# Kernel tuning notes

Hardware: AMD Instinct MI355X
Metric: run time of the kernel (lower is better)

The kernel has to match this reference:

```python
import jax, jax.numpy as jnp
import numpy as np

N_NODES = 100000
N_EDGES = 1200000
DIM = 64
MAX_DEG = 64
NUM_LAB = 16
BN_EPS = 1e-5


def _lrelu(x):
    return jax.nn.leaky_relu(x, negative_slope=0.01)


def _bn(x, g, b):
    # BatchNorm1d in training mode: batch statistics over node axis
    m = x.mean(axis=0)
    v = x.var(axis=0)
    return (x - m) * jax.lax.rsqrt(v + BN_EPS) * g + b


def _gin_layer(h, src, dst, n, w1, b1, w2, b2, eps, g, b):
    # GINConv: (1+eps)*x_i + sum_{j in N(i)} x_j, then MLP (lin_lrelu_lin), BN, LeakyReLU
    agg = jax.ops.segment_sum(h[src], dst, num_segments=n)
    x = (1.0 + eps) * h + agg
    x = _lrelu(x @ w1 + b1) @ w2 + b2
    return _lrelu(_bn(x, g, b))


def setup_inputs() -> dict:
    key = jax.random.key(0)
    ks = jax.random.split(key, 16)
    s = 0.05
    inp = {
        'node_deg': jax.random.randint(ks[0], (N_NODES,), 0, MAX_DEG + 1, dtype=jnp.int32),
        'node_lab': jax.random.randint(ks[1], (N_NODES,), 0, NUM_LAB, dtype=jnp.int32),
        'edge_index': jax.random.randint(ks[2], (2, N_EDGES), 0, N_NODES, dtype=jnp.int32),
        'emb_deg': jax.random.normal(ks[3], (MAX_DEG + 1, DIM), jnp.float32) * s,
        'emb_lab': jax.random.normal(ks[4], (NUM_LAB, DIM), jnp.float32) * s,
        'l0_w1': jax.random.normal(ks[5], (2 * DIM, 2 * DIM), jnp.float32) * s,
        'l0_b1': jnp.zeros((2 * DIM,), jnp.float32),
        'l0_w2': jax.random.normal(ks[6], (2 * DIM, DIM), jnp.float32) * s,
        'l0_b2': jnp.zeros((DIM,), jnp.float32),
        'l0_eps': jnp.zeros((1,), jnp.float32),
        'bn0_g': jnp.ones((DIM,), jnp.float32),
        'bn0_b': jnp.zeros((DIM,), jnp.float32),
        'l1_w1': jax.random.normal(ks[7], (DIM, DIM), jnp.float32) * s,
        'l1_b1': jnp.zeros((DIM,), jnp.float32),
        'l1_w2': jax.random.normal(ks[8], (DIM, DIM), jnp.float32) * s,
        'l1_b2': jnp.zeros((DIM,), jnp.float32),
        'l1_eps': jnp.zeros((1,), jnp.float32),
        'bn1_g': jnp.ones((DIM,), jnp.float32),
        'bn1_b': jnp.zeros((DIM,), jnp.float32),
        'fc_w1': jax.random.normal(ks[9], (4 * DIM, DIM), jnp.float32) * s,
        'fc_b1': jnp.zeros((DIM,), jnp.float32),
        'fc_bn_g': jnp.ones((DIM,), jnp.float32),
        'fc_bn_b': jnp.zeros((DIM,), jnp.float32),
        'fc_w2': jax.random.normal(ks[10], (DIM, 1), jnp.float32) * s,
        'fc_b2': jnp.zeros((1,), jnp.float32),
    }
    return inp


def reference(node_deg, node_lab, edge_index, emb_deg, emb_lab,
              l0_w1, l0_b1, l0_w2, l0_b2, l0_eps, bn0_g, bn0_b,
              l1_w1, l1_b1, l1_w2, l1_b2, l1_eps, bn1_g, bn1_b,
              fc_w1, fc_b1, fc_bn_g, fc_bn_b, fc_w2, fc_b2):
    n = node_deg.shape[0]
    src, dst = edge_index[0], edge_index[1]
    # embedding concat: [N, 2*DIM]
    h0 = jnp.concatenate([emb_deg[node_deg], emb_lab[node_lab]], axis=1)
    h1 = _gin_layer(h0, src, dst, n, l0_w1, l0_b1, l0_w2, l0_b2, l0_eps[0], bn0_g, bn0_b)
    h2 = _gin_layer(h1, src, dst, n, l1_w1, l1_b1, l1_w2, l1_b2, l1_eps[0], bn1_g, bn1_b)
    x = jnp.concatenate([h0, h1, h2], axis=1)  # [N, 256]
    x = _lrelu(_bn(x @ fc_w1 + fc_b1, fc_bn_g, fc_bn_b))
    out = jax.nn.sigmoid(x @ fc_w2 + fc_b2)
    return out.squeeze(-1)  # [N]
```

## Files before the change

### kernel.cpp

```cpp
#include <hip/hip_runtime.h>

#define N_NODES 100000
#define N_EDGES 1200000
#define NCLS 81
#define NBKT 196
#define BCAP 8192
#define NCHK 293
#define NGBLK 1563

typedef unsigned short u16;
typedef unsigned char u8;
typedef unsigned int u32;
typedef unsigned long long u64;
typedef short bf16x8 __attribute__((ext_vector_type(8)));
typedef float f32x4 __attribute__((ext_vector_type(4)));

__device__ __forceinline__ float b2f(u16 u) {
  union { u32 i; float f; } v; v.i = ((u32)u) << 16; return v.f;
}
__device__ __forceinline__ u16 f2b(float f) {
  union { float f; u32 i; } v; v.f = f;
  u32 x = v.i;
  return (u16)((x + 0x7fffu + ((x >> 16) & 1u)) >> 16);
}
__device__ __forceinline__ void up2(u32 w, float& lo, float& hi) {
  union { u32 u; float f; } a, b;
  a.u = w << 16; b.u = w & 0xffff0000u;
  lo = a.f; hi = b.f;
}
__device__ __forceinline__ float lrelu(float x) { return x > 0.f ? x : 0.01f * x; }

__device__ __forceinline__ bool is_f32(const u16* emb) {
  int lane = threadIdx.x & 63;
  u32 e0 = (emb[lane * 2] >> 7) & 0xFF;
  u32 e1 = (emb[lane * 2 + 1] >> 7) & 0xFF;
  return __ballot((e0 >= 0x90) || (e1 >= 0x90)) != 0ull;
}

__device__ __forceinline__ float rdr(const void* p, int i, bool f32m) {
  return f32m ? ((const float*)p)[i] : b2f(((const u16*)p)[i]);
}

#define P_EMBD 0
#define P_EMBL 4160
#define P_W1A  5184
#define P_B1A  21568
#define P_W2A  21696
#define P_B2A  29888
#define P_EPS0 29952
#define P_G0   29953
#define P_BB0  30017
#define P_LW1  30081
#define P_LB1  34177
#define P_LW2  34241
#define P_LB2  38337
#define P_EPS1 38401
#define P_G1   38402
#define P_BB1  38466
#define P_FW1  38530
#define P_FB1  54914
#define P_FG   54978
#define P_FBB  55042
#define P_FW2  55106
#define P_FB2  55170
#define P_TOT  55171

struct CvtAll {
  const void* src[22];
  int cnt[22];
  int off[22];
};

struct RawPtrs {
  const void* embD;
  const void* embL;
  const void* w1r;
  const void* w2r;
  const void* lw1r;
  const void* lw2r;
  const void* fwr;
};

__global__ void k_init(CvtAll a, RawPtrs rw, const u16* __restrict__ embRaw,
                       float* __restrict__ P, float* __restrict__ W1p,
                       float* __restrict__ Efc, u16* __restrict__ bp,
                       u16* __restrict__ wpB, u32* __restrict__ gcur) {
  bool f32m = is_f32(embRaw);
  int tid = threadIdx.x;
  if (blockIdx.y < 22) {
    if (blockIdx.y == 0 && blockIdx.x == 0 && tid < NBKT) gcur[tid] = 0;
    int seg = blockIdx.y;
    int i = blockIdx.x * 256 + tid;
    if (i < a.cnt[seg]) {
      float v = f32m ? ((const float*)a.src[seg])[i] : b2f(((const u16*)a.src[seg])[i]);
      P[a.off[seg] + i] = v;
    }
    return;
  }
  int idx = blockIdx.x * 256 + tid;
  if (idx < NCLS * 128) {
    int c = idx >> 7, h = idx & 127;
    float s = 0.f;
    if (c < 65) {
      for (int k = 0; k < 64; ++k)
        s = fmaf(rdr(rw.embD, c * 64 + k, f32m), rdr(rw.w1r, k * 128 + h, f32m), s);
    } else {
      for (int k = 0; k < 64; ++k)
        s = fmaf(rdr(rw.embL, (c - 65) * 64 + k, f32m), rdr(rw.w1r, (64 + k) * 128 + h, f32m), s);
    }
    W1p[idx] = s;
    return;
  }
  if (idx < NCLS * 128 + NCLS * 64) {
    int r = idx - NCLS * 128;
    int c = r >> 6, o = r & 63;
    float s = 0.f;
    if (c < 65) {
      for (int k = 0; k < 64; ++k)
        s = fmaf(rdr(rw.embD, c * 64 + k, f32m), rdr(rw.fwr, k * 64 + o, f32m), s);
    } else {
      for (int k = 0; k < 64; ++k)
        s = fmaf(rdr(rw.embL, (c - 65) * 64 + k, f32m), rdr(rw.fwr, (64 + k) * 64 + o, f32m), s);
    }
    Efc[r] = s;
    return;
  }
  if (idx < NCLS * 128 + NCLS * 64 + 24576) {
    int pidx = idx - (NCLS * 128 + NCLS * 64);
    int seg, rel;
    if (pidx < 8192)       { seg = 0; rel = pidx; }
    else if (pidx < 12288) { seg = 1; rel = pidx - 8192; }
    else if (pidx < 16384) { seg = 2; rel = pidx - 12288; }
    else                   { seg = 3; rel = pidx - 16384; }
    const void* srcs[4] = {rw.w2r, rw.lw1r, rw.lw2r, rw.fwr};
    const int addoff[4] = {0, 0, 0, 128 * 64};
    const int KBs[4] = {4, 2, 2, 4};
    int j = rel & 7, lane = (rel >> 3) & 63, rest = rel >> 9;
    int kb = rest % KBs[seg], nt = rest / KBs[seg];
    int k = kb * 32 + (lane >> 4) * 8 + j;
    int n = nt * 16 + (lane & 15);
    bp[pidx] = f2b(rdr(srcs[seg], addoff[seg] + k * 64 + n, f32m));
    return;
  }
  int p2 = idx - (NCLS * 128 + NCLS * 64 + 24576);
  if (p2 >= 12288) return;
  int j = p2 & 7, lane = (p2 >> 3) & 63, rest = p2 >> 9;
  int kb = rest % 3, nt = rest / 3;
  int c = kb * 32 + (lane >> 4) * 8 + j;
  int n = nt * 16 + (lane & 15);
  float s = 0.f;
  if (c < NCLS) {
    if (c < 65) {
      for (int k = 0; k < 64; ++k)
        s = fmaf(rdr(rw.embD, c * 64 + k, f32m), rdr(rw.w1r, k * 128 + n, f32m), s);
    } else {
      for (int k = 0; k < 64; ++k)
        s = fmaf(rdr(rw.embL, (c - 65) * 64 + k, f32m), rdr(rw.w1r, (64 + k) * 128 + n, f32m), s);
    }
  }
  wpB[p2] = (c < NCLS) ? f2b(s) : 0;
}

__global__ __launch_bounds__(256) void k_bsort(const int* __restrict__ edge,
                                               const int* __restrict__ ndeg,
                                               const int* __restrict__ nlab,
                                               u32* __restrict__ gcur,
                                               u64* __restrict__ e2) {
  __shared__ u32 cnt[NBKT], rbase[NBKT];
  __shared__ u32 slo[4096], shi[4096];
  for (int i = threadIdx.x; i < NBKT; i += 256) cnt[i] = 0;
  __syncthreads();
  int base = blockIdx.x * 4096;
  for (int i = threadIdx.x; i < 4096; i += 256) {
    int e = base + i;
    if (e < N_EDGES) {
      int s = edge[e], d = edge[N_EDGES + e];
      slo[i] = ((u32)s << 11) | ((u32)ndeg[s] << 4) | (u32)nlab[s];
      shi[i] = (u32)d;
      atomicAdd(&cnt[(u32)d >> 9], 1u);
    } else shi[i] = 0xFFFFFFFFu;
  }
  __syncthreads();
  for (int i = threadIdx.x; i < NBKT; i += 256) {
    u32 c = cnt[i];
    rbase[i] = c ? atomicAdd(&gcur[i], c) : 0u;
    cnt[i] = 0;
  }
  __syncthreads();
  for (int i = threadIdx.x; i < 4096; i += 256) {
    u32 d = shi[i];
    if (d == 0xFFFFFFFFu) continue;
    u32 b = d >> 9;
    u32 pos = rbase[b] + atomicAdd(&cnt[b], 1u);
    e2[(size_t)b * BCAP + pos] = ((u64)d << 32) | (u64)slo[i];
  }
}

__global__ __launch_bounds__(512) void k_csrh(const u64* __restrict__ e2,
                                              const u32* __restrict__ gcur,
                                              const u16* __restrict__ wpB,
                                              const float* __restrict__ W1p,
                                              const float* __restrict__ P,
                                              const int* __restrict__ ndeg,
                                              const int* __restrict__ nlab,
                                              u32* __restrict__ row_ptr,
                                              u32* __restrict__ einfo,
                                              u16* __restrict__ hmid) {
  __shared__ u32 l[512], cur[512], gl[NBKT];
  __shared__ u32 h32[512 * 24];
  __shared__ u32 sbase;
  int b = blockIdx.x, tid = threadIdx.x;
  if (tid < NBKT) gl[tid] = gcur[tid];
  l[tid] = 0;
  for (int i = tid; i < 512 * 24; i += 512) h32[i] = 0;
  __syncthreads();
  if (tid == 0) {
    u32 s = 0;
    for (int i = 0; i < b; ++i) s += gl[i];
    sbase = s;
  }
  __syncthreads();
  u32 cnt = gl[b];
  const u64* src = e2 + (size_t)b * BCAP;
  for (u32 e = tid; e < cnt; e += 512)
    atomicAdd(&l[(u32)(src[e] >> 32) & 511u], 1u);
  __syncthreads();
  u32 v = l[tid];
  for (int off = 1; off < 512; off <<= 1) {
    u32 a = (tid >= off) ? l[tid - off] : 0u;
    __syncthreads();
    l[tid] += a;
    __syncthreads();
  }
  u32 pos0 = sbase + l[tid] - v;
  cur[tid] = pos0;
  int nn = b * 512 + tid;
  if (nn <= N_NODES) row_ptr[nn] = pos0;
  __syncthreads();
  for (u32 e = tid; e < cnt; e += 512) {
    u64 r = src[e];
    u32 dl = (u32)(r >> 32) & 511u;
    u32 lo = (u32)r;
    u32 pos = atomicAdd(&cur[dl], 1u);
    einfo[pos] = lo;
    u32 c1 = (lo >> 4) & 0x7Fu, c2 = 65u + (lo & 15u);
    atomicAdd(&h32[dl * 24 + (c1 >> 2)], 1u << ((c1 & 3u) * 8));
    atomicAdd(&h32[dl * 24 + (c2 >> 2)], 1u << ((c2 & 3u) * 8));
  }
  __syncthreads();
  const u8* h = (const u8*)h32;
  int wid = tid >> 6, lane = tid & 63;
  int row = lane & 15, q = lane >> 4;
  float onep = 1.f + P[P_EPS0];
  const bf16x8* bp = (const bf16x8*)wpB;
#pragma unroll 1
  for (int t = wid; t < 32; t += 8) {
    int m0 = b * 512 + t * 16;
    if (m0 >= N_NODES) break;
    f32x4 acc[8];
#pragma unroll
    for (int nt = 0; nt < 8; ++nt) {
      float bb = P[P_B1A + nt * 16 + row];
      acc[nt][0] = bb; acc[nt][1] = bb; acc[nt][2] = bb; acc[nt][3] = bb;
    }
    const u8* ar = h + (t * 16 + row) * 96 + q * 8;
#pragma unroll
    for (int kb = 0; kb < 3; ++kb) {
      bf16x8 af;
#pragma unroll
      for (int j = 0; j < 8; ++j) af[j] = (short)f2b((float)ar[kb * 32 + j]);
#pragma unroll
      for (int nt = 0; nt < 8; ++nt) {
        bf16x8 bf = bp[(nt * 3 + kb) * 64 + lane];
        acc[nt] = __builtin_amdgcn_mfma_f32_16x16x32_bf16(af, bf, acc[nt], 0, 0, 0);
      }
    }
#pragma unroll
    for (int r = 0; r < 4; ++r) {
      int m = m0 + q * 4 + r;
      if (m >= N_NODES) continue;
      const float* wd = W1p + ndeg[m] * 128;
      const float* wl = W1p + (65 + nlab[m]) * 128;
#pragma unroll
      for (int nt = 0; nt < 8; ++nt) {
        int cc = nt * 16 + row;
        float vv = acc[nt][r] + onep * (wd[cc] + wl[cc]);
        hmid[(size_t)m * 128 + cc] = f2b(lrelu(vv));
      }
    }
  }
}

__global__ void k_sr(const float* __restrict__ pbuf, float* __restrict__ statsOut) {
  __shared__ float l[256];
  int c = blockIdx.x;
  float s = 0.f;
  for (int r = threadIdx.x; r < NGBLK; r += 256) s += pbuf[(size_t)r * 128 + c];
  l[threadIdx.x] = s;
  __syncthreads();
  for (int off = 128; off > 0; off >>= 1) {
    if (threadIdx.x < off) l[threadIdx.x] += l[threadIdx.x + off];
    __syncthreads();
  }
  if (threadIdx.x == 0) statsOut[c] = l[0];
}

template <int KB, int LDA, int BIASOFF>
__global__ __launch_bounds__(256) void k_gemm(const u16* __restrict__ A,
                                              const u16* __restrict__ Bp,
                                              const float* __restrict__ P,
                                              float* __restrict__ pbuf,
                                              u16* __restrict__ C) {
  __shared__ float lsum[4][64], lsq[4][64];
  int wid = threadIdx.x >> 6, lane = threadIdx.x & 63;
  int m0 = (blockIdx.x * 4 + wid) * 16;
  bool act = m0 < N_NODES;
  int row = lane & 15, q = lane >> 4;
  float ss[4] = {0.f, 0.f, 0.f, 0.f}, qq[4] = {0.f, 0.f, 0.f, 0.f};
  if (act) {
    const u16* ap = A + (size_t)(m0 + row) * LDA + q * 8;
    const bf16x8* bp = (const bf16x8*)Bp;
    f32x4 acc[4];
#pragma unroll
    for (int nt = 0; nt < 4; ++nt) {
      float b = (BIASOFF >= 0) ? P[BIASOFF + nt * 16 + row] : 0.f;
      acc[nt][0] = b; acc[nt][1] = b; acc[nt][2] = b; acc[nt][3] = b;
    }
#pragma unroll
    for (int kb = 0; kb < KB; ++kb) {
      bf16x8 af = *(const bf16x8*)(ap + kb * 32);
#pragma unroll
      for (int nt = 0; nt < 4; ++nt) {
        bf16x8 bf = bp[(nt * KB + kb) * 64 + lane];
        acc[nt] = __builtin_amdgcn_mfma_f32_16x16x32_bf16(af, bf, acc[nt], 0, 0, 0);
      }
    }
#pragma unroll
    for (int nt = 0; nt < 4; ++nt) {
      float s = 0.f, z = 0.f;
#pragma unroll
      for (int r = 0; r < 4; ++r) {
        int m = m0 + q * 4 + r;
        u16 bv = f2b(acc[nt][r]);
        C[(size_t)m * 64 + nt * 16 + row] = bv;
        float v = b2f(bv);
        s += v; z = fmaf(v, v, z);
      }
      s += __shfl_xor(s, 16, 64); s += __shfl_xor(s, 32, 64);
      z += __shfl_xor(z, 16, 64); z += __shfl_xor(z, 32, 64);
      ss[nt] = s; qq[nt] = z;
    }
  }
  if (lane < 16) {
#pragma unroll
    for (int nt = 0; nt < 4; ++nt) {
      lsum[wid][nt * 16 + lane] = ss[nt];
      lsq[wid][nt * 16 + lane] = qq[nt];
    }
  }
  __syncthreads();
  int t = threadIdx.x;
  if (t < 64)
    pbuf[(size_t)blockIdx.x * 128 + t] = lsum[0][t] + lsum[1][t] + lsum[2][t] + lsum[3][t];
  else if (t < 128) {
    int c = t - 64;
    pbuf[(size_t)blockIdx.x * 128 + t] = lsq[0][c] + lsq[1][c] + lsq[2][c] + lsq[3][c];
  }
}

__global__ __launch_bounds__(256) void k_gemm_bn(const u16* __restrict__ A,
                                                 const u16* __restrict__ Bp,
                                                 const float* __restrict__ P,
                                                 const float* __restrict__ stats,
                                                 u16* __restrict__ C) {
  int wid = threadIdx.x >> 6, lane = threadIdx.x & 63;
  int m0 = (blockIdx.x * 4 + wid) * 16;
  if (m0 >= N_NODES) return;
  int row = lane & 15, q = lane >> 4;
  const float invN = 1.f / (float)N_NODES;
  float sc[16], sh[16];
#pragma unroll
  for (int kb = 0; kb < 2; ++kb)
#pragma unroll
    for (int j = 0; j < 8; ++j) {
      int f = kb * 32 + q * 8 + j;
      float mm = stats[f] * invN;
      float var = fmaxf(stats[64 + f] * invN - mm * mm, 0.f);
      float inv = rsqrtf(var + 1e-5f);
      float s = inv * P[P_G0 + f];
      sc[kb * 8 + j] = s;
      sh[kb * 8 + j] = P[P_BB0 + f] - mm * s;
    }
  const u16* ap = A + (size_t)(m0 + row) * 64 + q * 8;
  const bf16x8* bp = (const bf16x8*)Bp;
  f32x4 acc[4];
#pragma unroll
  for (int nt = 0; nt < 4; ++nt) {
    acc[nt][0] = 0.f; acc[nt][1] = 0.f; acc[nt][2] = 0.f; acc[nt][3] = 0.f;
  }
#pragma unroll
  for (int kb = 0; kb < 2; ++kb) {
    uint4 raw = *(const uint4*)(ap + kb * 32);
    u32 rw[4] = {raw.x, raw.y, raw.z, raw.w};
    bf16x8 af;
#pragma unroll
    for (int p = 0; p < 4; ++p) {
      float lo, hi;
      up2(rw[p], lo, hi);
      float y0 = lrelu(fmaf(sc[kb * 8 + 2 * p], lo, sh[kb * 8 + 2 * p]));
      float y1 = lrelu(fmaf(sc[kb * 8 + 2 * p + 1], hi, sh[kb * 8 + 2 * p + 1]));
      af[2 * p] = (short)f2b(y0);
      af[2 * p + 1] = (short)f2b(y1);
    }
#pragma unroll
    for (int nt = 0; nt < 4; ++nt) {
      bf16x8 bf = bp[(nt * 2 + kb) * 64 + lane];
      acc[nt] = __builtin_amdgcn_mfma_f32_16x16x32_bf16(af, bf, acc[nt], 0, 0, 0);
    }
  }
#pragma unroll
  for (int nt = 0; nt < 4; ++nt)
#pragma unroll
    for (int r = 0; r < 4; ++r) {
      int m = m0 + q * 4 + r;
      C[(size_t)m * 64 + nt * 16 + row] = f2b(acc[nt][r]);
    }
}

__global__ __launch_bounds__(256) void k_agg_gemm(const u32* __restrict__ rp,
                                                  const u32* __restrict__ einfo,
                                                  const u16* __restrict__ g1,
                                                  const u16* __restrict__ Bp,
                                                  const float* __restrict__ P,
                                                  float* __restrict__ pbuf,
                                                  u16* __restrict__ C) {
  __shared__ float lsum[4][64], lsq[4][64];
  __shared__ u16 As[4][16][72];
  int wid = threadIdx.x >> 6, lane = threadIdx.x & 63;
  int m0 = (blockIdx.x * 4 + wid) * 16;
  bool act = m0 < N_NODES;
  int row = lane & 15, q = lane >> 4;
  float ss[4] = {0.f, 0.f, 0.f, 0.f}, qq[4] = {0.f, 0.f, 0.f, 0.f};
  if (act) {
    int grp = lane >> 4;
    int fo = (lane & 15) * 4;
    float onep = 1.f + P[P_EPS1];
    u32 rpv = 0;
    if (lane <= 16) rpv = rp[m0 + lane];
#pragma unroll 1
    for (int r = 0; r < 16; ++r) {
      int n = m0 + r;
      u32 st = (u32)__shfl((int)rpv, r, 64);
      u32 en = (u32)__shfl((int)rpv, r + 1, 64);
      u32 m = en - st;
      u32 myidx = (u32)n;
      if (lane < (int)m) myidx = einfo[st + lane] >> 11;
      u32 mm = m < 64u ? m : 64u;
      float a0 = 0.f, a1 = 0.f, a2 = 0.f, a3 = 0.f;
      for (u32 k = 0; k < mm; k += 16) {
#pragma unroll
        for (int bb = 0; bb < 4; ++bb) {
          u32 e = k + (u32)(bb * 4 + grp);
          u32 src = (u32)__shfl((int)myidx, (int)e, 64);
          if (e < mm) {
            uint2 v = *(const uint2*)(g1 + (size_t)src * 64 + fo);
            float l0, h0, l1, h1;
            up2(v.x, l0, h0);
            up2(v.y, l1, h1);
            a0 += l0; a1 += h0; a2 += l1; a3 += h1;
          }
        }
      }
      a0 += __shfl_xor(a0, 16, 64); a0 += __shfl_xor(a0, 32, 64);
      a1 += __shfl_xor(a1, 16, 64); a1 += __shfl_xor(a1, 32, 64);
      a2 += __shfl_xor(a2, 16, 64); a2 += __shfl_xor(a2, 32, 64);
      a3 += __shfl_xor(a3, 16, 64); a3 += __shfl_xor(a3, 32, 64);
      for (u32 k = 64; k < m; ++k) {
        u32 src = einfo[st + k] >> 11;
        uint2 v = *(const uint2*)(g1 + (size_t)src * 64 + fo);
        float l0, h0, l1, h1;
        up2(v.x, l0, h0);
        up2(v.y, l1, h1);
        a0 += l0; a1 += h0; a2 += l1; a3 += h1;
      }
      uint2 sv = *(const uint2*)(g1 + (size_t)n * 64 + fo);
      float s0, s1, s2, s3;
      up2(sv.x, s0, s1);
      up2(sv.y, s2, s3);
      float r0 = P[P_LB1 + fo + 0] + fmaf(onep, s0, a0);
      float r1 = P[P_LB1 + fo + 1] + fmaf(onep, s1, a1);
      float r2 = P[P_LB1 + fo + 2] + fmaf(onep, s2, a2);
      float r3 = P[P_LB1 + fo + 3] + fmaf(onep, s3, a3);
      if (lane < 16) {
        uint2 o;
        o.x = ((u32)f2b(lrelu(r0))) | (((u32)f2b(lrelu(r1))) << 16);
        o.y = ((u32)f2b(lrelu(r2))) | (((u32)f2b(lrelu(r3))) << 16);
        *(uint2*)&As[wid][r][fo] = o;
      }
    }
    const u16* ap = &As[wid][row][q * 8];
    const bf16x8* bp = (const bf16x8*)Bp;
    f32x4 acc[4];
#pragma unroll
    for (int nt = 0; nt < 4; ++nt) {
      float b = P[P_LB2 + nt * 16 + row];
      acc[nt][0] = b; acc[nt][1] = b; acc[nt][2] = b; acc[nt][3] = b;
    }
#pragma unroll
    for (int kb = 0; kb < 2; ++kb) {
      bf16x8 af = *(const bf16x8*)(ap + kb * 32);
#pragma unroll
      for (int nt = 0; nt < 4; ++nt) {
        bf16x8 bf = bp[(nt * 2 + kb) * 64 + lane];
        acc[nt] = __builtin_amdgcn_mfma_f32_16x16x32_bf16(af, bf, acc[nt], 0, 0, 0);
      }
    }
#pragma unroll
    for (int nt = 0; nt < 4; ++nt) {
      float s = 0.f, z = 0.f;
#pragma unroll
      for (int r = 0; r < 4; ++r) {
        int m = m0 + q * 4 + r;
        u16 bv = f2b(acc[nt][r]);
        C[(size_t)m * 64 + nt * 16 + row] = bv;
        float v = b2f(bv);
        s += v; z = fmaf(v, v, z);
      }
      s += __shfl_xor(s, 16, 64); s += __shfl_xor(s, 32, 64);
      z += __shfl_xor(z, 16, 64); z += __shfl_xor(z, 32, 64);
      ss[nt] = s; qq[nt] = z;
    }
  }
  if (lane < 16) {
#pragma unroll
    for (int nt = 0; nt < 4; ++nt) {
      lsum[wid][nt * 16 + lane] = ss[nt];
      lsq[wid][nt * 16 + lane] = qq[nt];
    }
  }
  __syncthreads();
  int t = threadIdx.x;
  if (t < 64)
    pbuf[(size_t)blockIdx.x * 128 + t] = lsum[0][t] + lsum[1][t] + lsum[2][t] + lsum[3][t];
  else if (t < 128) {
    int c = t - 64;
    pbuf[(size_t)blockIdx.x * 128 + t] = lsq[0][c] + lsq[1][c] + lsq[2][c] + lsq[3][c];
  }
}

__global__ __launch_bounds__(256) void k_gemm_fc1bn(const u16* __restrict__ t0,
                                                    const u16* __restrict__ t1,
                                                    const u16* __restrict__ Bp,
                                                    const float* __restrict__ P,
                                                    const float* __restrict__ stats,
                                                    float* __restrict__ pbuf,
                                                    const int* __restrict__ ndeg,
                                                    const int* __restrict__ nlab,
                                                    const float* __restrict__ Efc,
                                                    u16* __restrict__ C) {
  __shared__ float lsum[4][64], lsq[4][64];
  int wid = threadIdx.x >> 6, lane = threadIdx.x & 63;
  int m0 = (blockIdx.x * 4 + wid) * 16;
  bool act = m0 < N_NODES;
  int row = lane & 15, q = lane >> 4;
  float ss[4] = {0.f, 0.f, 0.f, 0.f}, qq[4] = {0.f, 0.f, 0.f, 0.f};
  if (act) {
    const float invN = 1.f / (float)N_NODES;
    float sc[32], sh[32];
#pragma unroll
    for (int h = 0; h < 2; ++h) {
      const float* st = stats + h * 128;
      int gof = h ? P_G1 : P_G0, bof = h ? P_BB1 : P_BB0;
#pragma unroll
      for (int kb = 0; kb < 2; ++kb)
#pragma unroll
        for (int j = 0; j < 8; ++j) {
          int f = kb * 32 + q * 8 + j;
          float mm = st[f] * invN;
          float var = fmaxf(st[64 + f] * invN - mm * mm, 0.f);
          float inv = rsqrtf(var + 1e-5f);
          float s = inv * P[gof + f];
          sc[h * 16 + kb * 8 + j] = s;
          sh[h * 16 + kb * 8 + j] = P[bof + f] - mm * s;
        }
    }
    const u16* a0 = t0 + (size_t)(m0 + row) * 64 + q * 8;
    const u16* a1 = t1 + (size_t)(m0 + row) * 64 + q * 8;
    const bf16x8* bp = (const bf16x8*)Bp;
    f32x4 acc[4];
#pragma unroll
    for (int nt = 0; nt < 4; ++nt) {
      float b = P[P_FB1 + nt * 16 + row];
      acc[nt][0] = b; acc[nt][1] = b; acc[nt][2] = b; acc[nt][3] = b;
    }
#pragma unroll
    for (int kb = 0; kb < 4; ++kb) {
      const u16* src = (kb < 2) ? (a0 + kb * 32) : (a1 + (kb - 2) * 32);
      int ci = (kb < 2) ? kb * 8 : 16 + (kb - 2) * 8;
      uint4 raw = *(const uint4*)src;
      u32 rw[4] = {raw.x, raw.y, raw.z, raw.w};
      bf16x8 af;
#pragma unroll
      for (int p = 0; p < 4; ++p) {
        float lo, hi;
        up2(rw[p], lo, hi);
        float y0 = lrelu(fmaf(sc[ci + 2 * p], lo, sh[ci + 2 * p]));
        float y1 = lrelu(fmaf(sc[ci + 2 * p + 1], hi, sh[ci + 2 * p + 1]));
        af[2 * p] = (short)f2b(y0);
        af[2 * p + 1] = (short)f2b(y1);
      }
#pragma unroll
      for (int nt = 0; nt < 4; ++nt) {
        bf16x8 bf = bp[(nt * 4 + kb) * 64 + lane];
        acc[nt] = __builtin_amdgcn_mfma_f32_16x16x32_bf16(af, bf, acc[nt], 0, 0, 0);
      }
    }
    float es[4][4];
#pragma unroll
    for (int r = 0; r < 4; ++r) {
      int m = m0 + q * 4 + r;
      int dn = ndeg[m], ln = 65 + nlab[m];
#pragma unroll
      for (int nt = 0; nt < 4; ++nt) {
        int cc = nt * 16 + row;
        es[r][nt] = acc[nt][r] + Efc[dn * 64 + cc] + Efc[ln * 64 + cc];
      }
    }
#pragma unroll
    for (int nt = 0; nt < 4; ++nt) {
      float s = 0.f, z = 0.f;
#pragma unroll
      for (int r = 0; r < 4; ++r) {
        int m = m0 + q * 4 + r;
        u16 bv = f2b(es[r][nt]);
        C[(size_t)m * 64 + nt * 16 + row] = bv;
        float v = b2f(bv);
        s += v; z = fmaf(v, v, z);
      }
      s += __shfl_xor(s, 16, 64); s += __shfl_xor(s, 32, 64);
      z += __shfl_xor(z, 16, 64); z += __shfl_xor(z, 32, 64);
      ss[nt] = s; qq[nt] = z;
    }
  }
  if (lane < 16) {
#pragma unroll
    for (int nt = 0; nt < 4; ++nt) {
      lsum[wid][nt * 16 + lane] = ss[nt];
      lsq[wid][nt * 16 + lane] = qq[nt];
    }
  }
  __syncthreads();
  int t = threadIdx.x;
  if (t < 64)
    pbuf[(size_t)blockIdx.x * 128 + t] = lsum[0][t] + lsum[1][t] + lsum[2][t] + lsum[3][t];
  else if (t < 128) {
    int c = t - 64;
    pbuf[(size_t)blockIdx.x * 128 + t] = lsq[0][c] + lsq[1][c] + lsq[2][c] + lsq[3][c];
  }
}

__global__ void k_fc2(const u16* __restrict__ t, const float* __restrict__ stats,
                      const float* __restrict__ P, const u16* __restrict__ embRaw,
                      void* __restrict__ out) {
  bool f32m = is_f32(embRaw);
  int n = blockIdx.x * blockDim.x + threadIdx.x;
  if (n >= N_NODES) return;
  float z = P[P_FB2];
  const float invN = 1.f / (float)N_NODES;
  const u16* tn = t + (size_t)n * 64;
#pragma unroll 1
  for (int f = 0; f < 64; ++f) {
    float m = stats[f] * invN;
    float var = fmaxf(stats[64 + f] * invN - m * m, 0.f);
    float inv = rsqrtf(var + 1e-5f);
    float y = (b2f(tn[f]) - m) * inv * P[P_FG + f] + P[P_FBB + f];
    y = lrelu(y);
    z = fmaf(y, P[P_FW2 + f], z);
  }
  float s = 1.f / (1.f + expf(-z));
  if (!(fabsf(z) < 1e30f)) s = 0.25f;
  if (f32m) ((float*)out)[n] = s;
  else      ((u16*)out)[n] = f2b(s);
}

extern "C" void kernel_launch(void* const* d_in, const int* in_sizes, int n_in,
                              void* d_out, int out_size, void* d_ws, size_t ws_size,
                              hipStream_t stream) {
  const int* node_deg = (const int*)d_in[0];
  const int* node_lab = (const int*)d_in[1];
  const int* edge     = (const int*)d_in[2];
  const u16* embRaw   = (const u16*)d_in[3];
  (void)in_sizes; (void)n_in; (void)out_size; (void)ws_size;

  char* base = (char*)d_ws;
  size_t off = 0;
  auto alloc = [&](size_t bytes) -> void* {
    void* p = base + off;
    off += (bytes + 15) & ~(size_t)15;
    return p;
  };
  float* Pb    = (float*)alloc((size_t)P_TOT * 4);
  float* stats = (float*)alloc(384 * 4);
  u32* gcur    = (u32*)alloc(NBKT * 4);
  float* W1p   = (float*)alloc(NCLS * 128 * 4);
  float* Efc   = (float*)alloc(NCLS * 64 * 4);
  u16* bpack   = (u16*)alloc(24576 * 2);
  u16* wpB     = (u16*)alloc(12288 * 2);
  u32* row_ptr = (u32*)alloc((size_t)(N_NODES + 1) * 4);
  float* pbuf  = (float*)alloc((size_t)NGBLK * 128 * 4);
  u32* einfo   = (u32*)alloc((size_t)N_EDGES * 4);
  u64* e2      = (u64*)alloc((size_t)NBKT * BCAP * 8);
  void* arena  = alloc((size_t)N_NODES * 128 * 2);
  u16* t0      = (u16*)alloc((size_t)N_NODES * 64 * 2);
  u16* t1      = (u16*)alloc((size_t)N_NODES * 64 * 2);
  u16* t2      = (u16*)alloc((size_t)N_NODES * 64 * 2);
  u16* hmid = (u16*)arena;
  u16* g1   = (u16*)arena;
  u16* Bp_w2a = bpack;
  u16* Bp_lw1 = bpack + 8192;
  u16* Bp_lw2 = bpack + 12288;
  u16* Bp_fw1 = bpack + 16384;

  CvtAll ca;
  const int srcidx[22] = {3, 4, 5, 6, 7, 8, 9, 10, 11, 12, 13, 14, 15, 16, 17, 18, 19, 20, 21, 22, 23, 24};
  const int cnts[22]   = {4160, 1024, 16384, 128, 8192, 64, 1, 64, 64, 4096, 64, 4096, 64, 1, 64, 64, 16384, 64, 64, 64, 64, 1};
  const int offs[22]   = {P_EMBD, P_EMBL, P_W1A, P_B1A, P_W2A, P_B2A, P_EPS0, P_G0, P_BB0,
                          P_LW1, P_LB1, P_LW2, P_LB2, P_EPS1, P_G1, P_BB1,
                          P_FW1, P_FB1, P_FG, P_FBB, P_FW2, P_FB2};
  for (int i = 0; i < 22; ++i) { ca.src[i] = d_in[srcidx[i]]; ca.cnt[i] = cnts[i]; ca.off[i] = offs[i]; }
  RawPtrs rw;
  rw.embD = d_in[3]; rw.embL = d_in[4]; rw.w1r = d_in[5]; rw.w2r = d_in[7];
  rw.lw1r = d_in[12]; rw.lw2r = d_in[14]; rw.fwr = d_in[19];

  k_init<<<dim3(205, 23), 256, 0, stream>>>(ca, rw, embRaw, Pb, W1p, Efc, bpack, wpB, gcur);

  k_bsort<<<NCHK, 256, 0, stream>>>(edge, node_deg, node_lab, gcur, e2);

  k_csrh<<<NBKT, 512, 0, stream>>>(e2, gcur, wpB, W1p, Pb, node_deg, node_lab,
                                   row_ptr, einfo, hmid);

  const int GEMM_GRID = NGBLK;

  k_gemm<4, 128, P_B2A><<<GEMM_GRID, 256, 0, stream>>>(hmid, Bp_w2a, Pb, pbuf, t0);
  k_sr<<<128, 256, 0, stream>>>(pbuf, stats);

  k_gemm_bn<<<GEMM_GRID, 256, 0, stream>>>(t0, Bp_lw1, Pb, stats, g1);
  k_agg_gemm<<<GEMM_GRID, 256, 0, stream>>>(row_ptr, einfo, g1, Bp_lw2, Pb, pbuf, t1);
  k_sr<<<128, 256, 0, stream>>>(pbuf, stats + 128);

  k_gemm_fc1bn<<<GEMM_GRID, 256, 0, stream>>>(t0, t1, Bp_fw1, Pb, stats, pbuf,
                                              node_deg, node_lab, Efc, t2);
  k_sr<<<128, 256, 0, stream>>>(pbuf, stats + 256);
  k_fc2<<<(N_NODES + 255) / 256, 256, 0, stream>>>(t2, stats + 256, Pb, embRaw, d_out);
}
```

Baseline: 340.7 us.

## Parallelize second-layer aggregation to one wave per node; hoist BN constants in fc2

The layer-1 aggregation+GEMM kernel previously had each wave serially walk 16 nodes' neighbor lists. Now each 1024-thread block assigns one wave per node, writes the aggregated rows to shared memory, and a single wave runs the MFMA and emits per-block BN partial sums. This gives more memory-level parallelism for the gather but leaves 15 waves idle during the GEMM and quadruples the partial-stats rows k_sr must reduce. Separately, k_fc2 precomputes the BN scale/shift and weights into shared memory per block and loads rows as vectorized uint4 instead of recomputing stats per feature per node.

```diff
diff --git a/kernel.cpp b/kernel.cpp
--- a/kernel.cpp
+++ b/kernel.cpp
@@ -7,6 +7,7 @@
 #define BCAP 8192
 #define NCHK 293
 #define NGBLK 1563
+#define NAGG 6250
 
 typedef unsigned short u16;
 typedef unsigned char u8;
@@ -291,11 +292,12 @@
   }
 }
 
-__global__ void k_sr(const float* __restrict__ pbuf, float* __restrict__ statsOut) {
+__global__ void k_sr(const float* __restrict__ pbuf, float* __restrict__ statsOut,
+                     int nrows) {
   __shared__ float l[256];
   int c = blockIdx.x;
   float s = 0.f;
-  for (int r = threadIdx.x; r < NGBLK; r += 256) s += pbuf[(size_t)r * 128 + c];
+  for (int r = threadIdx.x; r < nrows; r += 256) s += pbuf[(size_t)r * 128 + c];
   l[threadIdx.x] = s;
   __syncthreads();
   for (int off = 128; off > 0; off >>= 1) {
@@ -427,124 +429,108 @@
     }
 }
 
-__global__ __launch_bounds__(256) void k_agg_gemm(const u32* __restrict__ rp,
-                                                  const u32* __restrict__ einfo,
-                                                  const u16* __restrict__ g1,
-                                                  const u16* __restrict__ Bp,
-                                                  const float* __restrict__ P,
-                                                  float* __restrict__ pbuf,
-                                                  u16* __restrict__ C) {
-  __shared__ float lsum[4][64], lsq[4][64];
-  __shared__ u16 As[4][16][72];
-  int wid = threadIdx.x >> 6, lane = threadIdx.x & 63;
-  int m0 = (blockIdx.x * 4 + wid) * 16;
-  bool act = m0 < N_NODES;
-  int row = lane & 15, q = lane >> 4;
-  float ss[4] = {0.f, 0.f, 0.f, 0.f}, qq[4] = {0.f, 0.f, 0.f, 0.f};
-  if (act) {
-    int grp = lane >> 4;
-    int fo = (lane & 15) * 4;
-    float onep = 1.f + P[P_EPS1];
-    u32 rpv = 0;
-    if (lane <= 16) rpv = rp[m0 + lane];
-#pragma unroll 1
-    for (int r = 0; r < 16; ++r) {
-      int n = m0 + r;
-      u32 st = (u32)__shfl((int)rpv, r, 64);
-      u32 en = (u32)__shfl((int)rpv, r + 1, 64);
-      u32 m = en - st;
-      u32 myidx = (u32)n;
-      if (lane < (int)m) myidx = einfo[st + lane] >> 11;
-      u32 mm = m < 64u ? m : 64u;
-      float a0 = 0.f, a1 = 0.f, a2 = 0.f, a3 = 0.f;
-      for (u32 k = 0; k < mm; k += 16) {
-#pragma unroll
-        for (int bb = 0; bb < 4; ++bb) {
-          u32 e = k + (u32)(bb * 4 + grp);
-          u32 src = (u32)__shfl((int)myidx, (int)e, 64);
-          if (e < mm) {
-            uint2 v = *(const uint2*)(g1 + (size_t)src * 64 + fo);
-            float l0, h0, l1, h1;
-            up2(v.x, l0, h0);
-            up2(v.y, l1, h1);
-            a0 += l0; a1 += h0; a2 += l1; a3 += h1;
-          }
-        }
-      }
-      a0 += __shfl_xor(a0, 16, 64); a0 += __shfl_xor(a0, 32, 64);
-      a1 += __shfl_xor(a1, 16, 64); a1 += __shfl_xor(a1, 32, 64);
-      a2 += __shfl_xor(a2, 16, 64); a2 += __shfl_xor(a2, 32, 64);
-      a3 += __shfl_xor(a3, 16, 64); a3 += __shfl_xor(a3, 32, 64);
-      for (u32 k = 64; k < m; ++k) {
-        u32 src = einfo[st + k] >> 11;
+__global__ __launch_bounds__(1024) void k_aggg(const u32* __restrict__ rp,
+                                               const u32* __restrict__ einfo,
+                                               const u16* __restrict__ g1,
+                                               const u16* __restrict__ Bp,
+                                               const float* __restrict__ P,
+                                               float* __restrict__ pbuf,
+                                               u16* __restrict__ C) {
+  __shared__ u16 As[16][72];
+  int lane = threadIdx.x & 63, wv = threadIdx.x >> 6;
+  int m0 = blockIdx.x * 16;
+  int n = m0 + wv;
+  u32 st = rp[n], en = rp[n + 1];
+  u32 m = en - st;
+  int grp = lane >> 4;
+  int fo = (lane & 15) * 4;
+  u32 myidx = (u32)n;
+  if (lane < (int)m) myidx = einfo[st + lane] >> 11;
+  u32 mm = m < 64u ? m : 64u;
+  float a0 = 0.f, a1 = 0.f, a2 = 0.f, a3 = 0.f;
+  for (u32 k = 0; k < mm; k += 16) {
+#pragma unroll
+    for (int bb = 0; bb < 4; ++bb) {
+      u32 e = k + (u32)(bb * 4 + grp);
+      u32 src = (u32)__shfl((int)myidx, (int)e, 64);
+      if (e < mm) {
         uint2 v = *(const uint2*)(g1 + (size_t)src * 64 + fo);
         float l0, h0, l1, h1;
         up2(v.x, l0, h0);
         up2(v.y, l1, h1);
         a0 += l0; a1 += h0; a2 += l1; a3 += h1;
       }
-      uint2 sv = *(const uint2*)(g1 + (size_t)n * 64 + fo);
-      float s0, s1, s2, s3;
-      up2(sv.x, s0, s1);
-      up2(sv.y, s2, s3);
-      float r0 = P[P_LB1 + fo + 0] + fmaf(onep, s0, a0);
-      float r1 = P[P_LB1 + fo + 1] + fmaf(onep, s1, a1);
-      float r2 = P[P_LB1 + fo + 2] + fmaf(onep, s2, a2);
-      float r3 = P[P_LB1 + fo + 3] + fmaf(onep, s3, a3);
-      if (lane < 16) {
-        uint2 o;
-        o.x = ((u32)f2b(lrelu(r0))) | (((u32)f2b(lrelu(r1))) << 16);
-        o.y = ((u32)f2b(lrelu(r2))) | (((u32)f2b(lrelu(r3))) << 16);
-        *(uint2*)&As[wid][r][fo] = o;
-      }
-    }
-    const u16* ap = &As[wid][row][q * 8];
-    const bf16x8* bp = (const bf16x8*)Bp;
-    f32x4 acc[4];
-#pragma unroll
-    for (int nt = 0; nt < 4; ++nt) {
-      float b = P[P_LB2 + nt * 16 + row];
-      acc[nt][0] = b; acc[nt][1] = b; acc[nt][2] = b; acc[nt][3] = b;
-    }
-#pragma unroll
-    for (int kb = 0; kb < 2; ++kb) {
-      bf16x8 af = *(const bf16x8*)(ap + kb * 32);
-#pragma unroll
-      for (int nt = 0; nt < 4; ++nt) {
-        bf16x8 bf = bp[(nt * 2 + kb) * 64 + lane];
-        acc[nt] = __builtin_amdgcn_mfma_f32_16x16x32_bf16(af, bf, acc[nt], 0, 0, 0);
-      }
-    }
-#pragma unroll
-    for (int nt = 0; nt < 4; ++nt) {
-      float s = 0.f, z = 0.f;
-#pragma unroll
-      for (int r = 0; r < 4; ++r) {
-        int m = m0 + q * 4 + r;
-        u16 bv = f2b(acc[nt][r]);
-        C[(size_t)m * 64 + nt * 16 + row] = bv;
-        float v = b2f(bv);
-        s += v; z = fmaf(v, v, z);
-      }
-      s += __shfl_xor(s, 16, 64); s += __shfl_xor(s, 32, 64);
-      z += __shfl_xor(z, 16, 64); z += __shfl_xor(z, 32, 64);
-      ss[nt] = s; qq[nt] = z;
-    }
-  }
+    }
+  }
+  a0 += __shfl_xor(a0, 16, 64); a0 += __shfl_xor(a0, 32, 64);
+  a1 += __shfl_xor(a1, 16, 64); a1 += __shfl_xor(a1, 32, 64);
+  a2 += __shfl_xor(a2, 16, 64); a2 += __shfl_xor(a2, 32, 64);
+  a3 += __shfl_xor(a3, 16, 64); a3 += __shfl_xor(a3, 32, 64);
+  for (u32 k = 64; k < m; ++k) {
+    u32 src = einfo[st + k] >> 11;
+    uint2 v = *(const uint2*)(g1 + (size_t)src * 64 + fo);
+    float l0, h0, l1, h1;
+    up2(v.x, l0, h0);
+    up2(v.y, l1, h1);
+    a0 += l0; a1 += h0; a2 += l1; a3 += h1;
+  }
+  float onep = 1.f + P[P_EPS1];
+  uint2 sv = *(const uint2*)(g1 + (size_t)n * 64 + fo);
+  float s0, s1, s2, s3;
+  up2(sv.x, s0, s1);
+  up2(sv.y, s2, s3);
+  float r0 = P[P_LB1 + fo + 0] + fmaf(onep, s0, a0);
+  float r1 = P[P_LB1 + fo + 1] + fmaf(onep, s1, a1);
+  float r2 = P[P_LB1 + fo + 2] + fmaf(onep, s2, a2);
+  float r3 = P[P_LB1 + fo + 3] + fmaf(onep, s3, a3);
   if (lane < 16) {
-#pragma unroll
-    for (int nt = 0; nt < 4; ++nt) {
-      lsum[wid][nt * 16 + lane] = ss[nt];
-      lsq[wid][nt * 16 + lane] = qq[nt];
-    }
-  }
-  __syncthreads();
-  int t = threadIdx.x;
-  if (t < 64)
-    pbuf[(size_t)blockIdx.x * 128 + t] = lsum[0][t] + lsum[1][t] + lsum[2][t] + lsum[3][t];
-  else if (t < 128) {
-    int c = t - 64;
-    pbuf[(size_t)blockIdx.x * 128 + t] = lsq[0][c] + lsq[1][c] + lsq[2][c] + lsq[3][c];
+    uint2 o;
+    o.x = ((u32)f2b(lrelu(r0))) | (((u32)f2b(lrelu(r1))) << 16);
+    o.y = ((u32)f2b(lrelu(r2))) | (((u32)f2b(lrelu(r3))) << 16);
+    *(uint2*)&As[wv][fo] = o;
+  }
+  __syncthreads();
+  if (wv != 0) return;
+  int row = lane & 15, q = lane >> 4;
+  const u16* ap = &As[row][q * 8];
+  const bf16x8* bp = (const bf16x8*)Bp;
+  f32x4 acc[4];
+#pragma unroll
+  for (int nt = 0; nt < 4; ++nt) {
+    float b = P[P_LB2 + nt * 16 + row];
+    acc[nt][0] = b; acc[nt][1] = b; acc[nt][2] = b; acc[nt][3] = b;
+  }
+#pragma unroll
+  for (int kb = 0; kb < 2; ++kb) {
+    bf16x8 af = *(const bf16x8*)(ap + kb * 32);
+#pragma unroll
+    for (int nt = 0; nt < 4; ++nt) {
+      bf16x8 bf = bp[(nt * 2 + kb) * 64 + lane];
+      acc[nt] = __builtin_amdgcn_mfma_f32_16x16x32_bf16(af, bf, acc[nt], 0, 0, 0);
+    }
+  }
+  float ss[4], qq[4];
+#pragma unroll
+  for (int nt = 0; nt < 4; ++nt) {
+    float s = 0.f, z = 0.f;
+#pragma unroll
+    for (int r = 0; r < 4; ++r) {
+      int mo = m0 + q * 4 + r;
+      u16 bv = f2b(acc[nt][r]);
+      C[(size_t)mo * 64 + nt * 16 + row] = bv;
+      float v = b2f(bv);
+      s += v; z = fmaf(v, v, z);
+    }
+    s += __shfl_xor(s, 16, 64); s += __shfl_xor(s, 32, 64);
+    z += __shfl_xor(z, 16, 64); z += __shfl_xor(z, 32, 64);
+    ss[nt] = s; qq[nt] = z;
+  }
+  if (lane < 16) {
+#pragma unroll
+    for (int nt = 0; nt < 4; ++nt) {
+      pbuf[(size_t)blockIdx.x * 128 + nt * 16 + lane] = ss[nt];
+      pbuf[(size_t)blockIdx.x * 128 + 64 + nt * 16 + lane] = qq[nt];
+    }
   }
 }
 
@@ -659,23 +645,43 @@
   }
 }
 
-__global__ void k_fc2(const u16* __restrict__ t, const float* __restrict__ stats,
-                      const float* __restrict__ P, const u16* __restrict__ embRaw,
-                      void* __restrict__ out) {
+__global__ __launch_bounds__(256) void k_fc2(const u16* __restrict__ t,
+                                             const float* __restrict__ stats,
+                                             const float* __restrict__ P,
+                                             const u16* __restrict__ embRaw,
+                                             void* __restrict__ out) {
+  __shared__ float scF[64], shF[64], fwF[64];
   bool f32m = is_f32(embRaw);
-  int n = blockIdx.x * blockDim.x + threadIdx.x;
+  int tid = threadIdx.x;
+  if (tid < 64) {
+    const float invN = 1.f / (float)N_NODES;
+    float mm = stats[tid] * invN;
+    float var = fmaxf(stats[64 + tid] * invN - mm * mm, 0.f);
+    float inv = rsqrtf(var + 1e-5f);
+    float s = inv * P[P_FG + tid];
+    scF[tid] = s;
+    shF[tid] = P[P_FBB + tid] - mm * s;
+    fwF[tid] = P[P_FW2 + tid];
+  }
+  __syncthreads();
+  int n = blockIdx.x * 256 + tid;
   if (n >= N_NODES) return;
   float z = P[P_FB2];
-  const float invN = 1.f / (float)N_NODES;
-  const u16* tn = t + (size_t)n * 64;
-#pragma unroll 1
-  for (int f = 0; f < 64; ++f) {
-    float m = stats[f] * invN;
-    float var = fmaxf(stats[64 + f] * invN - m * m, 0.f);
-    float inv = rsqrtf(var + 1e-5f);
-    float y = (b2f(tn[f]) - m) * inv * P[P_FG + f] + P[P_FBB + f];
-    y = lrelu(y);
-    z = fmaf(y, P[P_FW2 + f], z);
+  const uint4* tn = (const uint4*)(t + (size_t)n * 64);
+#pragma unroll
+  for (int jj = 0; jj < 8; ++jj) {
+    uint4 raw = tn[jj];
+    u32 w[4] = {raw.x, raw.y, raw.z, raw.w};
+#pragma unroll
+    for (int p = 0; p < 4; ++p) {
+      int f = jj * 8 + p * 2;
+      float lo, hi;
+      up2(w[p], lo, hi);
+      float y0 = lrelu(fmaf(scF[f], lo, shF[f]));
+      float y1 = lrelu(fmaf(scF[f + 1], hi, shF[f + 1]));
+      z = fmaf(y0, fwF[f], z);
+      z = fmaf(y1, fwF[f + 1], z);
+    }
   }
   float s = 1.f / (1.f + expf(-z));
   if (!(fabsf(z) < 1e30f)) s = 0.25f;
@@ -707,7 +713,7 @@
   u16* bpack   = (u16*)alloc(24576 * 2);
   u16* wpB     = (u16*)alloc(12288 * 2);
   u32* row_ptr = (u32*)alloc((size_t)(N_NODES + 1) * 4);
-  float* pbuf  = (float*)alloc((size_t)NGBLK * 128 * 4);
+  float* pbuf  = (float*)alloc((size_t)NAGG * 128 * 4);
   u32* einfo   = (u32*)alloc((size_t)N_EDGES * 4);
   u64* e2      = (u64*)alloc((size_t)NBKT * BCAP * 8);
   void* arena  = alloc((size_t)N_NODES * 128 * 2);
@@ -742,14 +748,14 @@
   const int GEMM_GRID = NGBLK;
 
   k_gemm<4, 128, P_B2A><<<GEMM_GRID, 256, 0, stream>>>(hmid, Bp_w2a, Pb, pbuf, t0);
-  k_sr<<<128, 256, 0, stream>>>(pbuf, stats);
+  k_sr<<<128, 256, 0, stream>>>(pbuf, stats, NGBLK);
 
   k_gemm_bn<<<GEMM_GRID, 256, 0, stream>>>(t0, Bp_lw1, Pb, stats, g1);
-  k_agg_gemm<<<GEMM_GRID, 256, 0, stream>>>(row_ptr, einfo, g1, Bp_lw2, Pb, pbuf, t1);
-  k_sr<<<128, 256, 0, stream>>>(pbuf, stats + 128);
+  k_aggg<<<NAGG, 1024, 0, stream>>>(row_ptr, einfo, g1, Bp_lw2, Pb, pbuf, t1);
+  k_sr<<<128, 256, 0, stream>>>(pbuf, stats + 128, NAGG);
 
   k_gemm_fc1bn<<<GEMM_GRID, 256, 0, stream>>>(t0, t1, Bp_fw1, Pb, stats, pbuf,
                                               node_deg, node_lab, Efc, t2);
-  k_sr<<<128, 256, 0, stream>>>(pbuf, stats + 256);
+  k_sr<<<128, 256, 0, stream>>>(pbuf, stats + 256, NGBLK);
   k_fc2<<<(N_NODES + 255) / 256, 256, 0, stream>>>(t2, stats + 256, Pb, embRaw, d_out);
 }
```

Result: faster. 331.3 us (-2.8%).
